# Performance work log

Hardware: AMD Instinct MI355X
Metric: run time of the kernel (lower is better)

The kernel has to match this reference:

```python
import jax, jax.numpy as jnp
import numpy as np
from jax import lax

N = 16384          # total nodes
NUM_GRAPHS = 256   # graphs in the batch
K = 50             # self.knn
NUM_BINS = 5       # num_edge_features
RDF_CUTOFF = 10.0  # Angstrom-scale cutoff for Gaussian RDF smearing
BIG = 1e10         # masked-distance sentinel (finite, jit-safe)


def setup_inputs() -> dict:
    key = jax.random.key(0)
    k1, k2 = jax.random.split(key)
    # 3D pharmacophore coordinates, ~Angstrom scale
    pos = jax.random.normal(k1, (N, 3), dtype=jnp.float32) * 3.0
    # sorted graph-id vector (PyG `batch`)
    batch = jnp.sort(jax.random.randint(k2, (N,), 0, NUM_GRAPHS, dtype=jnp.int64))
    return {"pos": pos, "batch": batch}


def reference(pos, batch):
    n = pos.shape[0]
    # --- brute-force KNN graph (T.KNNGraph, per-graph via batch mask) ---
    sq = jnp.sum(pos * pos, axis=-1)                         # [n]
    d2 = sq[:, None] + sq[None, :] - 2.0 * (pos @ pos.T)     # [n, n]
    same_graph = batch[:, None] == batch[None, :]
    valid = same_graph & ~jnp.eye(n, dtype=bool)             # no self-loops
    d2m = jnp.where(valid, d2, BIG)
    neg_d2, nbr_idx = lax.top_k(-d2m, K)                     # [n, K] nearest by distance
    # symmetric-superset edge list: j -> i (source_to_target flow)
    src = nbr_idx.reshape(-1)                                # [n*K]
    dst = jnp.repeat(jnp.arange(n), K)                       # [n*K]
    edge_index = jnp.stack([src, dst])                       # [2, n*K]
    # --- T.Distance(norm=False): raw Euclidean edge lengths ---
    dist = jnp.sqrt(jnp.maximum(-neg_d2, 1e-12)).reshape(-1)  # [n*K]
    # --- DistanceRDF(num_bins): Gaussian smearing of distances over bins ---
    centers = jnp.linspace(0.0, RDF_CUTOFF, NUM_BINS, dtype=pos.dtype)
    spacing = RDF_CUTOFF / (NUM_BINS - 1)
    gamma = 1.0 / (2.0 * spacing * spacing)
    rdf = jnp.exp(-gamma * (dist[:, None] - centers[None, :]) ** 2)  # [n*K, NUM_BINS]
    return edge_index, dist, rdf
```

## Files before the change

kernel.cpp:

```cpp
#include <hip/hip_runtime.h>
#include <math.h>

#define NTOT  16384
#define NGR   256
#define KNN   50
#define NBINS 5
#define BIGF  1e10f
#define MAXJ  2

__global__ __launch_bounds__(256)
void bounds_kernel(const int* __restrict__ batch, int* __restrict__ bounds)
{
    const int i = blockIdx.x * 256 + threadIdx.x;
    if (i > NTOT) return;
    const int cur  = (i < NTOT) ? batch[i] : NGR;
    const int prev = (i == 0) ? -1 : batch[i - 1];
    for (int t = prev + 1; t <= cur; ++t) bounds[t] = i;
}

__device__ __forceinline__ unsigned int rdlane(unsigned int v, int l)
{
    return (unsigned int)__builtin_amdgcn_readlane((int)v, l);
}

template <int J>
__device__ __forceinline__ void rank_count(const unsigned long long (&key)[MAXJ],
                                           int (&rank)[MAXJ], int cnt)
{
    int ra[MAXJ] = {0, 0}, rb[MAXJ] = {0, 0};
    #pragma unroll
    for (int j2 = 0; j2 < J; ++j2) {
        const int base = j2 * 64;
        const int kmax = min(64, cnt - base);
        const int kpad = (kmax + 7) & ~7;
        const unsigned int mlo = (unsigned int)key[j2];
        const unsigned int mhi = (unsigned int)(key[j2] >> 32);
        for (int k0 = 0; k0 < kpad; k0 += 8) {
            #pragma unroll
            for (int u = 0; u < 8; ++u) {
                const unsigned int lo = rdlane(mlo, k0 + u);
                const unsigned int hi = rdlane(mhi, k0 + u);
                const unsigned long long kk = ((unsigned long long)hi << 32) | lo;
                #pragma unroll
                for (int j = 0; j < J; ++j) {
                    if (u & 1) rb[j] += (kk < key[j]);
                    else       ra[j] += (kk < key[j]);
                }
            }
        }
    }
    #pragma unroll
    for (int j = 0; j < J; ++j) rank[j] = ra[j] + rb[j];
}

__global__ __launch_bounds__(256)
void knn_main(const float* __restrict__ pos,
              const int*   __restrict__ batch,
              const int*   __restrict__ bounds,
              float*       __restrict__ out)
{
    const int i    = __builtin_amdgcn_readfirstlane((int)(blockIdx.x * 4 + (threadIdx.x >> 6)));
    const int lane = threadIdx.x & 63;

    const int g     = batch[i];
    const int start = bounds[g];
    const int end   = bounds[g + 1];
    const int cnt   = end - start;
    const int J     = (cnt + 63) >> 6;

    const float xi = pos[(size_t)i * 3 + 0];
    const float yi = pos[(size_t)i * 3 + 1];
    const float zi = pos[(size_t)i * 3 + 2];
    const float sqi = xi * xi + yi * yi + zi * zi;

    unsigned long long key[MAXJ];
    #pragma unroll
    for (int j = 0; j < MAXJ; ++j) {
        const int c = j * 64 + lane;
        float d2 = BIGF;
        if (j < J && c < cnt && (start + c) != i) {
            const int idx = start + c;
            const float xj = pos[(size_t)idx * 3 + 0];
            const float yj = pos[(size_t)idx * 3 + 1];
            const float zj = pos[(size_t)idx * 3 + 2];
            const float sqj = xj * xj + yj * yj + zj * zj;
            const float dot = xi * xj + yi * yj + zi * zj;
            d2 = sqi + sqj - 2.0f * dot;
        }
        const unsigned int b = __float_as_uint(d2);
        const unsigned int s = ((int)b < 0) ? ~b : (b | 0x80000000u);
        key[j] = ((unsigned long long)s << 32) | (unsigned int)(start + c);
    }

    int rank[MAXJ] = {0, 0};
    if (J == 1) rank_count<1>(key, rank, cnt);
    else        rank_count<2>(key, rank, cnt);

    float* __restrict__ srcO  = out;
    float* __restrict__ dstO  = out + (size_t)NTOT * KNN;
    float* __restrict__ distO = out + (size_t)2 * NTOT * KNN;
    float* __restrict__ rdfO  = out + (size_t)3 * NTOT * KNN;

    const float centers[NBINS] = {0.0f, 2.5f, 5.0f, 7.5f, 10.0f};
    const float gamma = 0.08f;
    const float fi = (float)i;

    #pragma unroll
    for (int j = 0; j < MAXJ; ++j) {
        const int c = j * 64 + lane;
        if (j < J && c < cnt && (start + c) != i && rank[j] < KNN) {
            const unsigned int s  = (unsigned int)(key[j] >> 32);
            const unsigned int b  = (s & 0x80000000u) ? (s & 0x7fffffffu) : ~s;
            const float d2 = __uint_as_float(b);
            const size_t e = (size_t)i * KNN + rank[j];
            srcO[e]  = (float)(start + c);
            dstO[e]  = fi;
            const float d = sqrtf(fmaxf(d2, 1e-12f));
            distO[e] = d;
            #pragma unroll
            for (int bb = 0; bb < NBINS; ++bb) {
                const float dd = d - centers[bb];
                rdfO[e * NBINS + bb] = __expf(-gamma * dd * dd);
            }
        }
    }

    if (cnt <= KNN) {
        const int r = (cnt - 1) + lane;
        if (r < KNN) {
            const int m = lane;
            int jj;
            if (m < start)       jj = m;
            else if (m == start) jj = i;
            else                 jj = end + (m - start - 1);
            const size_t e = (size_t)i * KNN + r;
            srcO[e]  = (float)jj;
            dstO[e]  = fi;
            distO[e] = 100000.0f;
            #pragma unroll
            for (int bb = 0; bb < NBINS; ++bb)
                rdfO[e * NBINS + bb] = 0.0f;
        }
    }
}

extern "C" void kernel_launch(void* const* d_in, const int* in_sizes, int n_in,
                              void* d_out, int out_size, void* d_ws, size_t ws_size,
                              hipStream_t stream) {
    const float* pos    = (const float*)d_in[0];
    const int*   batch  = (const int*)d_in[1];
    float*       out    = (float*)d_out;
    int*         bounds = (int*)d_ws;

    bounds_kernel<<<dim3(65), dim3(256), 0, stream>>>(batch, bounds);
    knn_main<<<dim3(NTOT / 4), dim3(256), 0, stream>>>(pos, batch, bounds, out);
}
```

Baseline: 83.60 us.

## Split KNN into rank kernel writing packed records and coalesced expand kernel

The ranking kernel now writes a compact (index, squared-distance bits) record per edge into workspace instead of scattering all outputs. A separate expand kernel, with one thread per edge, reads the records and writes src, dst, dist and the RDF bins. The goal is coalesced output stores in place of the scattered per-rank writes. The cost is an extra launch and a round trip through an 8 MB intermediate buffer. The padding path now stores BIG and gets the distance from sqrt, so it yields 1e5 as before but the RDF bins become exp of a large negative (about 0) rather than an explicit 0.

Result: slower. 86.85 us (+3.9%).

```diff
diff --git a/kernel.cpp b/kernel.cpp
--- a/kernel.cpp
+++ b/kernel.cpp
@@ -54,10 +54,10 @@
 }
 
 __global__ __launch_bounds__(256)
-void knn_main(const float* __restrict__ pos,
+void knn_rank(const float* __restrict__ pos,
               const int*   __restrict__ batch,
               const int*   __restrict__ bounds,
-              float*       __restrict__ out)
+              uint2*       __restrict__ rec)
 {
     const int i    = __builtin_amdgcn_readfirstlane((int)(blockIdx.x * 4 + (threadIdx.x >> 6)));
     const int lane = threadIdx.x & 63;
@@ -96,32 +96,13 @@
     if (J == 1) rank_count<1>(key, rank, cnt);
     else        rank_count<2>(key, rank, cnt);
 
-    float* __restrict__ srcO  = out;
-    float* __restrict__ dstO  = out + (size_t)NTOT * KNN;
-    float* __restrict__ distO = out + (size_t)2 * NTOT * KNN;
-    float* __restrict__ rdfO  = out + (size_t)3 * NTOT * KNN;
-
-    const float centers[NBINS] = {0.0f, 2.5f, 5.0f, 7.5f, 10.0f};
-    const float gamma = 0.08f;
-    const float fi = (float)i;
-
     #pragma unroll
     for (int j = 0; j < MAXJ; ++j) {
         const int c = j * 64 + lane;
         if (j < J && c < cnt && (start + c) != i && rank[j] < KNN) {
             const unsigned int s  = (unsigned int)(key[j] >> 32);
             const unsigned int b  = (s & 0x80000000u) ? (s & 0x7fffffffu) : ~s;
-            const float d2 = __uint_as_float(b);
-            const size_t e = (size_t)i * KNN + rank[j];
-            srcO[e]  = (float)(start + c);
-            dstO[e]  = fi;
-            const float d = sqrtf(fmaxf(d2, 1e-12f));
-            distO[e] = d;
-            #pragma unroll
-            for (int bb = 0; bb < NBINS; ++bb) {
-                const float dd = d - centers[bb];
-                rdfO[e * NBINS + bb] = __expf(-gamma * dd * dd);
-            }
+            rec[(size_t)i * KNN + rank[j]] = make_uint2((unsigned int)(start + c), b);
         }
     }
 
@@ -133,14 +114,34 @@
             if (m < start)       jj = m;
             else if (m == start) jj = i;
             else                 jj = end + (m - start - 1);
-            const size_t e = (size_t)i * KNN + r;
-            srcO[e]  = (float)jj;
-            dstO[e]  = fi;
-            distO[e] = 100000.0f;
-            #pragma unroll
-            for (int bb = 0; bb < NBINS; ++bb)
-                rdfO[e * NBINS + bb] = 0.0f;
+            rec[(size_t)i * KNN + r] = make_uint2((unsigned int)jj, __float_as_uint(BIGF));
         }
+    }
+}
+
+__global__ __launch_bounds__(256)
+void knn_expand(const uint2* __restrict__ rec, float* __restrict__ out)
+{
+    const int e = blockIdx.x * 256 + threadIdx.x;
+    const uint2 r = rec[e];
+
+    float* __restrict__ srcO  = out;
+    float* __restrict__ dstO  = out + (size_t)NTOT * KNN;
+    float* __restrict__ distO = out + (size_t)2 * NTOT * KNN;
+    float* __restrict__ rdfO  = out + (size_t)3 * NTOT * KNN;
+
+    const float centers[NBINS] = {0.0f, 2.5f, 5.0f, 7.5f, 10.0f};
+    const float gamma = 0.08f;
+
+    srcO[e] = (float)(int)r.x;
+    dstO[e] = (float)(e / KNN);
+    const float d2 = __uint_as_float(r.y);
+    const float d  = sqrtf(fmaxf(d2, 1e-12f));
+    distO[e] = d;
+    #pragma unroll
+    for (int b = 0; b < NBINS; ++b) {
+        const float dd = d - centers[b];
+        rdfO[(size_t)e * NBINS + b] = __expf(-gamma * dd * dd);
     }
 }
 
@@ -150,8 +151,10 @@
     const float* pos    = (const float*)d_in[0];
     const int*   batch  = (const int*)d_in[1];
     float*       out    = (float*)d_out;
-    int*         bounds = (int*)d_ws;
+    uint2*       rec    = (uint2*)d_ws;
+    int*         bounds = (int*)((char*)d_ws + (8u << 20));
 
-    bounds_kernel<<<dim3(65), dim3(256), 0, stream>>>(batch, bounds);
-    knn_main<<<dim3(NTOT / 4), dim3(256), 0, stream>>>(pos, batch, bounds, out);
+    bounds_kernel<<<dim3(65),   dim3(256), 0, stream>>>(batch, bounds);
+    knn_rank  <<<dim3(NTOT / 4), dim3(256), 0, stream>>>(pos, batch, bounds, rec);
+    knn_expand<<<dim3(NTOT * KNN / 256), dim3(256), 0, stream>>>(rec, out);
 }
```
